# Kernel optimization log

Measured on AMD Instinct MI355X. Metric: run time of the kernel, lower is better.

## Reference

```python
import jax, jax.numpy as jnp
import numpy as np
import math

D_MODEL = 1024
NUM_HEADS = 16
D_HEAD = D_MODEL // NUM_HEADS
BATCH = 2
SEQ = 2048


def setup_inputs() -> dict:
    key = jax.random.key(0)
    ks = jax.random.split(key, 5)
    sigma = math.sqrt(2.0 / (D_MODEL + D_MODEL))
    x = jax.random.normal(ks[0], (BATCH, SEQ, D_MODEL), dtype=jnp.float32)
    WQ = jax.random.normal(ks[1], (D_MODEL, D_MODEL), dtype=jnp.float32) * sigma
    WK = jax.random.normal(ks[2], (D_MODEL, D_MODEL), dtype=jnp.float32) * sigma
    WV = jax.random.normal(ks[3], (D_MODEL, D_MODEL), dtype=jnp.float32) * sigma
    WO = jax.random.normal(ks[4], (D_MODEL, D_MODEL), dtype=jnp.float32) * sigma
    return {"x": x, "WQ": WQ, "WK": WK, "WV": WV, "WO": WO}


def _softmax_fp32(scores):
    # matches custom softmax: compute in fp32, cast back to input dtype
    dtype = scores.dtype
    s = scores.astype(jnp.float32)
    return jax.nn.softmax(s, axis=-1).astype(dtype)


def reference(x, WQ, WK, WV, WO):
    batch, seq_len, _ = x.shape
    def split_heads(t):
        return t.reshape(batch, seq_len, NUM_HEADS, D_HEAD).transpose(0, 2, 1, 3)
    Q = split_heads(x @ WQ.T)  # [b,h,s,d]
    K = split_heads(x @ WK.T)
    V = split_heads(x @ WV.T)
    scale = 1.0 / math.sqrt(D_HEAD)
    scores = jnp.einsum('bhqd,bhkd->bhqk', Q, K) * scale
    # precomputed additive causal mask: 0 on/below diag, -inf above
    causal = jnp.triu(jnp.full((seq_len, seq_len), -jnp.inf, dtype=scores.dtype), k=1)
    scores = scores + causal
    attn = _softmax_fp32(scores)
    out = jnp.einsum('bhqk,bhkd->bhqd', attn, V)  # [b,h,s,d]
    out = out.transpose(0, 2, 1, 3).reshape(batch, seq_len, D_MODEL)
    return out @ WO.T
```

## Files before the change

### kernel.cpp

```cpp
#include <hip/hip_runtime.h>
#include <hip/hip_bf16.h>
#include <math.h>

typedef unsigned int u32;
typedef unsigned short u16;
typedef __attribute__((ext_vector_type(4))) float f32x4;
typedef __attribute__((ext_vector_type(4))) short bf16x4;
typedef __attribute__((ext_vector_type(8))) short bf16x8;
typedef __attribute__((ext_vector_type(4))) unsigned short u16x4;

#define D_MODEL 1024
#define SEQ     2048
#define NH      16
#define DH      64
#define MTOT    4096

#define QK_SCALE (0.125f * 1.44269504088896340736f)

__device__ __forceinline__ u16 f2bf(float f) {
  union { float f; u32 u; } a; a.f = f;
  u32 r = a.u + 0x7fffu + ((a.u >> 16) & 1u);
  return (u16)(r >> 16);
}

__device__ __forceinline__ void async_copy16(const void* g, void* l) {
  __builtin_amdgcn_global_load_lds(
      (const __attribute__((address_space(1))) u32*)g,
      (__attribute__((address_space(3))) u32*)l, 16, 0, 0);
}

__global__ __launch_bounds__(256) void k_convert(
    const float* __restrict__ x,  const float* __restrict__ wq,
    const float* __restrict__ wk, const float* __restrict__ wv,
    const float* __restrict__ wo,
    u16* __restrict__ xb,  u16* __restrict__ wqb, u16* __restrict__ wkb,
    u16* __restrict__ wvb, u16* __restrict__ wob) {
  const long NX = (long)MTOT * D_MODEL / 8;
  const long NW = (long)D_MODEL * D_MODEL / 8;
  long i = (long)blockIdx.x * 256 + threadIdx.x;
  const float* src; u16* dst;
  if (i < NX)               { src = x;  dst = xb;  }
  else if (i < NX + NW)     { src = wq; dst = wqb; i -= NX; }
  else if (i < NX + 2*NW)   { src = wk; dst = wkb; i -= NX + 2*NW - NW; }
  else if (i < NX + 3*NW)   { src = wv; dst = wvb; i -= NX + 2*NW; }
  else                      { src = wo; dst = wob; i -= NX + 3*NW; }
  const f32x4* s4 = (const f32x4*)src + i * 2;
  f32x4 a = s4[0], b = s4[1];
  union { bf16x8 v; u16 e[8]; } o;
  o.e[0] = f2bf(a[0]); o.e[1] = f2bf(a[1]); o.e[2] = f2bf(a[2]); o.e[3] = f2bf(a[3]);
  o.e[4] = f2bf(b[0]); o.e[5] = f2bf(b[1]); o.e[6] = f2bf(b[2]); o.e[7] = f2bf(b[3]);
  *(bf16x8*)(dst + i * 8) = o.v;
}

__device__ __forceinline__ void gemm_core(
    const u16* __restrict__ A, const u16* __restrict__ Bm,
    u16* As, u16* Bs, f32x4 acc[4][4], int m0, int n0) {
  const int t = threadIdx.x;
  const int lane = t & 63, w = t >> 6;
  const int wr = (w >> 1) * 64, wc = (w & 1) * 64;
  const int lr = lane & 15, g = lane >> 4;
  const int rr = t >> 2, c8 = (t & 3) * 8;
#pragma unroll
  for (int mi = 0; mi < 4; ++mi)
#pragma unroll
    for (int ni = 0; ni < 4; ++ni)
      acc[mi][ni] = (f32x4){0.f, 0.f, 0.f, 0.f};
  const u16* ga0 = A  + (size_t)(m0 + rr) * D_MODEL + c8;
  const u16* ga1 = A  + (size_t)(m0 + 64 + rr) * D_MODEL + c8;
  const u16* gb0 = Bm + (size_t)(n0 + rr) * D_MODEL + c8;
  const u16* gb1 = Bm + (size_t)(n0 + 64 + rr) * D_MODEL + c8;
  for (int k0 = 0; k0 < D_MODEL; k0 += 32) {
    async_copy16(ga0 + k0, As + t * 8);
    async_copy16(ga1 + k0, As + 2048 + t * 8);
    async_copy16(gb0 + k0, Bs + t * 8);
    async_copy16(gb1 + k0, Bs + 2048 + t * 8);
    __syncthreads();
    bf16x8 af[4], bfr[4];
#pragma unroll
    for (int mi = 0; mi < 4; ++mi)
      af[mi] = *(const bf16x8*)(As + (wr + mi * 16 + lr) * 32 + g * 8);
#pragma unroll
    for (int ni = 0; ni < 4; ++ni)
      bfr[ni] = *(const bf16x8*)(Bs + (wc + ni * 16 + lr) * 32 + g * 8);
#pragma unroll
    for (int mi = 0; mi < 4; ++mi)
#pragma unroll
      for (int ni = 0; ni < 4; ++ni)
        acc[mi][ni] = __builtin_amdgcn_mfma_f32_16x16x32_bf16(
            af[mi], bfr[ni], acc[mi][ni], 0, 0, 0);
    __syncthreads();
  }
}

__global__ __launch_bounds__(256) void k_gemm_qkv(
    const u16* __restrict__ xb, const u16* __restrict__ wqb,
    const u16* __restrict__ wkb, const u16* __restrict__ wvb,
    u16* __restrict__ Qo, u16* __restrict__ Ko, u16* __restrict__ Vt) {
  __shared__ u16 As[128 * 32], Bs[128 * 32];
  const int m0 = blockIdx.x * 128;
  const int n0g = blockIdx.y * 128;
  const int proj = n0g >> 10;
  const int n0 = n0g & 1023;
  const u16* Bm = (proj == 0) ? wqb : (proj == 1) ? wkb : wvb;
  const float scale = (proj == 0) ? QK_SCALE : 1.0f;
  f32x4 acc[4][4];
  gemm_core(xb, Bm, As, Bs, acc, m0, n0);
  const int t = threadIdx.x, lane = t & 63, w = t >> 6;
  const int wr = (w >> 1) * 64, wc = (w & 1) * 64;
  const int lr = lane & 15, g = lane >> 4;
  if (proj != 2) {
    u16* Out = (proj == 0) ? Qo : Ko;
#pragma unroll
    for (int mi = 0; mi < 4; ++mi)
#pragma unroll
      for (int ni = 0; ni < 4; ++ni)
#pragma unroll
        for (int jj = 0; jj < 4; ++jj) {
          int m = m0 + wr + mi * 16 + 4 * g + jj;
          int cn = n0 + wc + ni * 16 + lr;
          int h = cn >> 6, d = cn & 63;
          int b = m >> 11, s = m & 2047;
          Out[(((size_t)(b * NH + h) * SEQ) + s) * DH + d] =
              f2bf(acc[mi][ni][jj] * scale);
        }
  } else {
#pragma unroll
    for (int mi = 0; mi < 4; ++mi)
#pragma unroll
      for (int ni = 0; ni < 4; ++ni) {
        u16x4 pk;
#pragma unroll
        for (int jj = 0; jj < 4; ++jj) pk[jj] = f2bf(acc[mi][ni][jj]);
        int mb = m0 + wr + mi * 16 + 4 * g;
        int cn = n0 + wc + ni * 16 + lr;
        int h = cn >> 6, d = cn & 63;
        int b = mb >> 11, s = mb & 2047;
        *(u16x4*)(Vt + (((size_t)(b * NH + h) * DH + d) * SEQ) + s) = pk;
      }
  }
}

__global__ __launch_bounds__(256, 4) void k_attn(
    const u16* __restrict__ Q, const u16* __restrict__ K,
    const u16* __restrict__ Vt, u16* __restrict__ att) {
  __shared__ u16 Ksh[2][4096];
  __shared__ u16 Vsh[2][4096];
  const int t = threadIdx.x, lane = t & 63, w = t >> 6;
  const int lr = lane & 15, g = lane >> 4;
  const int bid = blockIdx.x;
  const int k4 = bid & 7;
  const int bh = (bid >> 3) & 31;
  const int j4 = bid >> 8;
  const int qb = (j4 == 0) ? k4 : (j4 == 1) ? (15 - k4)
               : (j4 == 2) ? (16 + k4) : (31 - k4);
  const int q0 = qb * 64, qw = q0 + w * 16;
  const size_t hb = (size_t)bh * SEQ * DH;
  const u16* Qp  = Q  + hb;
  const u16* Kp  = K  + hb;
  const u16* Vtp = Vt + hb;

  bf16x8 qfr[2];
#pragma unroll
  for (int kk = 0; kk < 2; ++kk)
    qfr[kk] = *(const bf16x8*)(Qp + (size_t)(qw + lr) * DH + kk * 32 + g * 8);

  f32x4 o[4];
#pragma unroll
  for (int d = 0; d < 4; ++d) o[d] = (f32x4){0.f, 0.f, 0.f, 0.f};
  float mrow = -__builtin_inff();
  float lrow = 0.f;

  const int sswz = ((t & 7) * 16) ^ (((t >> 3) & 7) << 4);
  const char* srcK = (const char*)Kp + (t >> 3) * 128 + sswz;
  const char* srcV = (const char*)Vtp + (t >> 3) * 4096 + sswz;

  const int nkv = qb + 1;
  int cur = 0;

  async_copy16(srcK,          (char*)&Ksh[0][0] + t * 16);
  async_copy16(srcK + 4096,   (char*)&Ksh[0][0] + 4096 + t * 16);
  async_copy16(srcV,          (char*)&Vsh[0][0] + t * 16);
  async_copy16(srcV + 131072, (char*)&Vsh[0][0] + 4096 + t * 16);

  for (int it = 0; it < nkv; ++it) {
    const int kv0 = it * 64;
    __syncthreads();
    if (it + 1 < nkv) {
      const char* sk = srcK + (size_t)(it + 1) * 8192;
      const char* sv = srcV + (size_t)(it + 1) * 128;
      char* kd = (char*)&Ksh[cur ^ 1][0];
      char* vd = (char*)&Vsh[cur ^ 1][0];
      async_copy16(sk,          kd + t * 16);
      async_copy16(sk + 4096,   kd + 4096 + t * 16);
      async_copy16(sv,          vd + t * 16);
      async_copy16(sv + 131072, vd + 4096 + t * 16);
    }
    if (kv0 <= qw + 15) {
      const char* kbase = (const char*)&Ksh[cur][0];
      const char* vbase = (const char*)&Vsh[cur][0];
      bf16x8 kfr[4][2];
#pragma unroll
      for (int mf = 0; mf < 4; ++mf) {
        int row = mf * 16 + lr;
#pragma unroll
        for (int kk = 0; kk < 2; ++kk) {
          int off = (row * 128 + kk * 64 + g * 16) ^ ((row & 7) << 4);
          kfr[mf][kk] = *(const bf16x8*)(kbase + off);
        }
      }
      f32x4 st[4];
#pragma unroll
      for (int mf = 0; mf < 4; ++mf) {
        f32x4 z = (f32x4){0.f, 0.f, 0.f, 0.f};
        z = __builtin_amdgcn_mfma_f32_16x16x32_bf16(kfr[mf][0], qfr[0], z, 0, 0, 0);
        st[mf] = __builtin_amdgcn_mfma_f32_16x16x32_bf16(kfr[mf][1], qfr[1], z, 0, 0, 0);
      }
      if (kv0 + 63 > qw) {
#pragma unroll
        for (int mf = 0; mf < 4; ++mf)
#pragma unroll
          for (int jj = 0; jj < 4; ++jj) {
            int kv = kv0 + mf * 16 + 4 * g + jj;
            st[mf][jj] = (kv > qw + lr) ? -__builtin_inff() : st[mf][jj];
          }
      }
      float v01 = fmaxf(fmaxf(fmaxf(st[0][0], st[0][1]), fmaxf(st[0][2], st[0][3])),
                        fmaxf(fmaxf(st[1][0], st[1][1]), fmaxf(st[1][2], st[1][3])));
      float v23 = fmaxf(fmaxf(fmaxf(st[2][0], st[2][1]), fmaxf(st[2][2], st[2][3])),
                        fmaxf(fmaxf(st[3][0], st[3][1]), fmaxf(st[3][2], st[3][3])));
      float v = fmaxf(v01, v23);
      v = fmaxf(v, __shfl_xor(v, 16));
      v = fmaxf(v, __shfl_xor(v, 32));
      float mnew = fmaxf(mrow, v);
      float fac = exp2f(mrow - mnew);
      mrow = mnew;
      float p[4][4];
      float sum = 0.f;
#pragma unroll
      for (int mf = 0; mf < 4; ++mf)
#pragma unroll
        for (int jj = 0; jj < 4; ++jj) {
          p[mf][jj] = exp2f(st[mf][jj] - mrow);
          sum += p[mf][jj];
        }
      sum += __shfl_xor(sum, 16);
      sum += __shfl_xor(sum, 32);
      lrow = lrow * fac + sum;
      float fq[4];
#pragma unroll
      for (int jj = 0; jj < 4; ++jj)
        fq[jj] = __shfl(fac, 4 * g + jj);
#pragma unroll
      for (int d = 0; d < 4; ++d)
#pragma unroll
        for (int jj = 0; jj < 4; ++jj)
          o[d][jj] *= fq[jj];
      bf16x8 pa[2];
#pragma unroll
      for (int ks = 0; ks < 2; ++ks)
#pragma unroll
        for (int m4 = 0; m4 < 2; ++m4)
#pragma unroll
          for (int jj = 0; jj < 4; ++jj)
            pa[ks][m4 * 4 + jj] = (short)f2bf(p[ks * 2 + m4][jj]);
#pragma unroll
      for (int ks = 0; ks < 2; ++ks) {
        bf16x8 vb[4];
#pragma unroll
        for (int dd = 0; dd < 4; ++dd) {
          int row = dd * 16 + lr;
          int sz = (row & 7) << 4;
          union { bf16x8 v8; bf16x4 h[2]; } u;
          u.h[0] = *(const bf16x4*)(vbase + ((row * 128 + ks * 64 + g * 8) ^ sz));
          u.h[1] = *(const bf16x4*)(vbase + ((row * 128 + ks * 64 + 32 + g * 8) ^ sz));
          vb[dd] = u.v8;
        }
#pragma unroll
        for (int dd = 0; dd < 4; ++dd)
          o[dd] = __builtin_amdgcn_mfma_f32_16x16x32_bf16(pa[ks], vb[dd], o[dd], 0, 0, 0);
      }
    }
    cur ^= 1;
  }
  float li[4];
#pragma unroll
  for (int jj = 0; jj < 4; ++jj)
    li[jj] = 1.0f / __shfl(lrow, 4 * g + jj);
  const int b = bh >> 4, h = bh & 15;
#pragma unroll
  for (int d = 0; d < 4; ++d)
#pragma unroll
    for (int jj = 0; jj < 4; ++jj) {
      int q = qw + 4 * g + jj;
      int cn = h * 64 + d * 16 + lr;
      att[(size_t)(b * SEQ + q) * D_MODEL + cn] = f2bf(o[d][jj] * li[jj]);
    }
}

__global__ __launch_bounds__(256) void k_gemm_out(
    const u16* __restrict__ att, const u16* __restrict__ wob,
    float* __restrict__ out) {
  __shared__ u16 As[128 * 32], Bs[128 * 32];
  const int m0 = blockIdx.x * 128, n0 = blockIdx.y * 128;
  f32x4 acc[4][4];
  gemm_core(att, wob, As, Bs, acc, m0, n0);
  const int t = threadIdx.x, lane = t & 63, w = t >> 6;
  const int wr = (w >> 1) * 64, wc = (w & 1) * 64;
  const int lr = lane & 15, g = lane >> 4;
#pragma unroll
  for (int mi = 0; mi < 4; ++mi)
#pragma unroll
    for (int ni = 0; ni < 4; ++ni)
#pragma unroll
      for (int jj = 0; jj < 4; ++jj) {
        int m = m0 + wr + mi * 16 + 4 * g + jj;
        int n = n0 + wc + ni * 16 + lr;
        out[(size_t)m * D_MODEL + n] = acc[mi][ni][jj];
      }
}

extern "C" void kernel_launch(void* const* d_in, const int* in_sizes, int n_in,
                              void* d_out, int out_size, void* d_ws, size_t ws_size,
                              hipStream_t stream) {
  (void)in_sizes; (void)n_in; (void)out_size; (void)ws_size;
  const float* x  = (const float*)d_in[0];
  const float* WQ = (const float*)d_in[1];
  const float* WK = (const float*)d_in[2];
  const float* WV = (const float*)d_in[3];
  const float* WO = (const float*)d_in[4];
  float* out = (float*)d_out;
  char* ws = (char*)d_ws;
  u16* xb  = (u16*)(ws);
  u16* wqb = (u16*)(ws + ((size_t)8 << 20));
  u16* wkb = (u16*)(ws + ((size_t)10 << 20));
  u16* wvb = (u16*)(ws + ((size_t)12 << 20));
  u16* wob = (u16*)(ws + ((size_t)14 << 20));
  u16* Qb  = (u16*)(ws + ((size_t)16 << 20));
  u16* Kb  = (u16*)(ws + ((size_t)24 << 20));
  u16* Vtb = (u16*)(ws + ((size_t)32 << 20));
  u16* att = (u16*)(ws + ((size_t)40 << 20));

  hipLaunchKernelGGL(k_convert, dim3(4096), dim3(256), 0, stream,
                     x, WQ, WK, WV, WO, xb, wqb, wkb, wvb, wob);
  hipLaunchKernelGGL(k_gemm_qkv, dim3(32, 24), dim3(256), 0, stream,
                     xb, wqb, wkb, wvb, Qb, Kb, Vtb);
  hipLaunchKernelGGL(k_attn, dim3(1024), dim3(256), 0, stream,
                     Qb, Kb, Vtb, att);
  hipLaunchKernelGGL(k_gemm_out, dim3(32, 8), dim3(256), 0, stream,
                     att, wob, out);
}
```

Measured before the change: 215.2 us.

## Lazy softmax rescale, MFMA row sums, packed bf16 convert, reorder q-block schedule

Reworks the attention softmax inner loop. The running max and output rescale now happen only when some row max grows by more than 8 (log2 units), and the row sums come from an MFMA of the bf16 probabilities against a ones vector instead of shuffles. Probability packing uses the hardware v_cvt_pk_bf16_f32 instruction, and the causal q-block ordering across the grid is permuted to balance work. The aim is fewer VALU ops, shuffles and rescale work per tile. In exchange, the denominator is summed from bf16-rounded probabilities and exponent values can reach 2^8 before a rescale.

```diff
diff --git a/kernel.cpp b/kernel.cpp
--- a/kernel.cpp
+++ b/kernel.cpp
@@ -21,6 +21,12 @@
   union { float f; u32 u; } a; a.f = f;
   u32 r = a.u + 0x7fffu + ((a.u >> 16) & 1u);
   return (u16)(r >> 16);
+}
+
+__device__ __forceinline__ u32 cvtpk(float lo, float hi) {
+  u32 r;
+  asm("v_cvt_pk_bf16_f32 %0, %1, %2" : "=v"(r) : "v"(lo), "v"(hi));
+  return r;
 }
 
 __device__ __forceinline__ void async_copy16(const void* g, void* l) {
@@ -151,8 +157,8 @@
   const int k4 = bid & 7;
   const int bh = (bid >> 3) & 31;
   const int j4 = bid >> 8;
-  const int qb = (j4 == 0) ? k4 : (j4 == 1) ? (15 - k4)
-               : (j4 == 2) ? (16 + k4) : (31 - k4);
+  const int qb = (j4 == 0) ? (31 - k4) : (j4 == 1) ? k4
+               : (j4 == 2) ? (23 - k4) : (8 + k4);
   const int q0 = qb * 64, qw = q0 + w * 16;
   const size_t hb = (size_t)bh * SEQ * DH;
   const u16* Qp  = Q  + hb;
@@ -167,8 +173,12 @@
   f32x4 o[4];
 #pragma unroll
   for (int d = 0; d < 4; ++d) o[d] = (f32x4){0.f, 0.f, 0.f, 0.f};
+  f32x4 lacc = (f32x4){0.f, 0.f, 0.f, 0.f};
   float mrow = -__builtin_inff();
-  float lrow = 0.f;
+
+  const short one_bf = (short)0x3F80;
+  const bf16x8 onesb = {one_bf, one_bf, one_bf, one_bf,
+                        one_bf, one_bf, one_bf, one_bf};
 
   const int sswz = ((t & 7) * 16) ^ (((t >> 3) & 7) << 4);
   const char* srcK = (const char*)Kp + (t >> 3) * 128 + sswz;
@@ -231,38 +241,41 @@
       float v = fmaxf(v01, v23);
       v = fmaxf(v, __shfl_xor(v, 16));
       v = fmaxf(v, __shfl_xor(v, 32));
-      float mnew = fmaxf(mrow, v);
-      float fac = exp2f(mrow - mnew);
-      mrow = mnew;
+      if (__any(v > mrow + 8.0f)) {
+        float mnew = fmaxf(mrow, v);
+        float fac = exp2f(mrow - mnew);
+        mrow = mnew;
+        float fq[4];
+#pragma unroll
+        for (int jj = 0; jj < 4; ++jj)
+          fq[jj] = __shfl(fac, 4 * g + jj);
+#pragma unroll
+        for (int d = 0; d < 4; ++d)
+#pragma unroll
+          for (int jj = 0; jj < 4; ++jj)
+            o[d][jj] *= fq[jj];
+#pragma unroll
+        for (int jj = 0; jj < 4; ++jj)
+          lacc[jj] *= fq[jj];
+      }
       float p[4][4];
-      float sum = 0.f;
 #pragma unroll
       for (int mf = 0; mf < 4; ++mf)
 #pragma unroll
-        for (int jj = 0; jj < 4; ++jj) {
+        for (int jj = 0; jj < 4; ++jj)
           p[mf][jj] = exp2f(st[mf][jj] - mrow);
-          sum += p[mf][jj];
-        }
-      sum += __shfl_xor(sum, 16);
-      sum += __shfl_xor(sum, 32);
-      lrow = lrow * fac + sum;
-      float fq[4];
-#pragma unroll
-      for (int jj = 0; jj < 4; ++jj)
-        fq[jj] = __shfl(fac, 4 * g + jj);
-#pragma unroll
-      for (int d = 0; d < 4; ++d)
-#pragma unroll
-        for (int jj = 0; jj < 4; ++jj)
-          o[d][jj] *= fq[jj];
       bf16x8 pa[2];
 #pragma unroll
-      for (int ks = 0; ks < 2; ++ks)
-#pragma unroll
-        for (int m4 = 0; m4 < 2; ++m4)
-#pragma unroll
-          for (int jj = 0; jj < 4; ++jj)
-            pa[ks][m4 * 4 + jj] = (short)f2bf(p[ks * 2 + m4][jj]);
+      for (int ks = 0; ks < 2; ++ks) {
+        union { bf16x8 v8; u32 wdz[4]; } pu;
+        pu.wdz[0] = cvtpk(p[ks * 2][0],     p[ks * 2][1]);
+        pu.wdz[1] = cvtpk(p[ks * 2][2],     p[ks * 2][3]);
+        pu.wdz[2] = cvtpk(p[ks * 2 + 1][0], p[ks * 2 + 1][1]);
+        pu.wdz[3] = cvtpk(p[ks * 2 + 1][2], p[ks * 2 + 1][3]);
+        pa[ks] = pu.v8;
+      }
+      lacc = __builtin_amdgcn_mfma_f32_16x16x32_bf16(pa[0], onesb, lacc, 0, 0, 0);
+      lacc = __builtin_amdgcn_mfma_f32_16x16x32_bf16(pa[1], onesb, lacc, 0, 0, 0);
 #pragma unroll
       for (int ks = 0; ks < 2; ++ks) {
         bf16x8 vb[4];
@@ -282,19 +295,17 @@
     }
     cur ^= 1;
   }
-  float li[4];
-#pragma unroll
-  for (int jj = 0; jj < 4; ++jj)
-    li[jj] = 1.0f / __shfl(lrow, 4 * g + jj);
   const int b = bh >> 4, h = bh & 15;
 #pragma unroll
-  for (int d = 0; d < 4; ++d)
-#pragma unroll
-    for (int jj = 0; jj < 4; ++jj) {
-      int q = qw + 4 * g + jj;
+  for (int jj = 0; jj < 4; ++jj) {
+    float li = 1.0f / lacc[jj];
+    int q = qw + 4 * g + jj;
+#pragma unroll
+    for (int d = 0; d < 4; ++d) {
       int cn = h * 64 + d * 16 + lr;
-      att[(size_t)(b * SEQ + q) * D_MODEL + cn] = f2bf(o[d][jj] * li[jj]);
+      att[(size_t)(b * SEQ + q) * D_MODEL + cn] = f2bf(o[d][jj] * li);
     }
+  }
 }
 
 __global__ __launch_bounds__(256) void k_gemm_out(
```

New measurement: 196.1 us. -8.9%, faster.
